# Kernel tuning notes

Hardware: AMD Instinct MI355X
Metric: run time of the kernel (lower is better)

Reference implementation:

```python
import jax, jax.numpy as jnp
import numpy as np


def _scan_dir(x, Wk, Wr, b):
    # x: (B,H,W,C) already flipped for the direction; Wk:(C,4U) Wr:(U,4U) b:(4U,)
    B, H, W, C = x.shape
    U = Wr.shape[0]
    Dmax = min(H, W)          # max anti-diagonal length
    D = H + W - 1             # number of anti-diagonals
    dt = x.dtype
    k = jnp.arange(Dmax)

    def step(carry, d):
        h1, c1, h2, c2 = carry            # diag d-1 and d-2 buffers, (B,Dmax,U)
        i0 = jnp.maximum(0, d - (W - 1))  # first row on diag d
        i1 = jnp.minimum(H - 1, d)        # last row on diag d
        rows = i0 + k
        cols = d - rows
        mask = rows <= i1                 # valid lanes on this diagonal
        rs = jnp.clip(rows, 0, H - 1)
        cs = jnp.clip(cols, 0, W - 1)
        x_diag = x[:, rs, cs, :]          # (B,Dmax,C)
        i0p = jnp.maximum(0, d - W)       # i0 of diag d-1
        i0pp = jnp.maximum(0, d - 1 - W)  # i0 of diag d-2

        def nb(buf, r_nb, lane0, extra):
            v = mask & extra
            lane = jnp.clip(r_nb - lane0, 0, Dmax - 1)
            g = jnp.take(buf, lane, axis=1)
            return jnp.where(v[None, :, None], g, jnp.zeros_like(g)), v

        up_ok = rows - 1 >= 0
        left_ok = cols - 1 >= 0
        h_up, v_up = nb(h1, rows - 1, i0p, up_ok)        # (i-1, j)   on diag d-1
        h_left, v_left = nb(h1, rows, i0p, left_ok)      # (i, j-1)   on diag d-1
        h_ul, v_ul = nb(h2, rows - 1, i0pp, up_ok & left_ok)  # (i-1,j-1) diag d-2
        c_up, _ = nb(c1, rows - 1, i0p, up_ok)
        c_left, _ = nb(c1, rows, i0p, left_ok)
        c_ul, _ = nb(c2, rows - 1, i0pp, up_ok & left_ok)

        cnt = (v_up.astype(dt) + v_left.astype(dt) + v_ul.astype(dt))[None, :, None]
        cnt = jnp.maximum(cnt, jnp.asarray(1.0, dt))
        h_prev = (h_up + h_left + h_ul) / cnt
        c_prev = (c_up + c_left + c_ul) / cnt

        # keras LSTMCell math, gate order i,f,g,o
        z = x_diag @ Wk + h_prev @ Wr + b
        zi, zf, zg, zo = jnp.split(z, 4, axis=-1)
        c_new = jax.nn.sigmoid(zf) * c_prev + jax.nn.sigmoid(zi) * jnp.tanh(zg)
        h_new = jax.nn.sigmoid(zo) * jnp.tanh(c_new)
        m = mask[None, :, None]
        h_new = jnp.where(m, h_new, jnp.zeros_like(h_new))
        c_new = jnp.where(m, c_new, jnp.zeros_like(c_new))
        return (h_new, c_new, h1, c1), h_new

    z0 = jnp.zeros((B, Dmax, U), dt)
    _, hs = jax.lax.scan(step, (z0, z0, z0, z0), jnp.arange(D))  # (D,B,Dmax,U)

    # scatter diagonal buffers back into the (B,H,W,U) grid (static indices)
    d_arr = np.arange(D)[:, None]
    kk = np.arange(Dmax)[None, :]
    rows_all = np.maximum(0, d_arr - (W - 1)) + kk
    cols_all = d_arr - rows_all
    valid = rows_all <= np.minimum(H - 1, d_arr)
    rws = np.where(valid, rows_all, H)   # invalid lanes -> padding row H
    cws = np.where(valid, cols_all, 0)
    out = jnp.zeros((B, H + 1, W, U), dt)
    out = out.at[:, rws, cws].set(jnp.transpose(hs, (1, 0, 2, 3)))
    return out[:, :H]


_FLIPS = [(False, False), (False, True), (True, False), (True, True)]  # SE,SW,NE,NW


def _forward(x, Wk, Wr, b):
    outs = []
    for i, (fh, fw) in enumerate(_FLIPS):
        xx = x
        if fh:
            xx = xx[:, ::-1]
        if fw:
            xx = xx[:, :, ::-1]
        o = _scan_dir(xx, Wk[i], Wr[i], b[i])
        if fw:
            o = o[:, :, ::-1]
        if fh:
            o = o[:, ::-1]
        outs.append(o)
    return jnp.concatenate(outs, axis=-1)


def setup_inputs() -> dict:
    key = jax.random.key(0)
    k0, k1, k2, k3 = jax.random.split(key, 4)
    B, H, W, C, U = 4, 128, 128, 64, 64
    x = jax.random.normal(k0, (B, H, W, C), jnp.float32)
    Wk = jax.random.normal(k1, (4, C, 4 * U), jnp.float32) * 0.08
    Wr = jax.random.normal(k2, (4, U, 4 * U), jnp.float32) * 0.08
    b = jax.random.normal(k3, (4, 4 * U), jnp.float32) * 0.02
    return {"x": x, "Wk": Wk, "Wr": Wr, "b": b}


def reference(x, Wk, Wr, b):
    return _forward(x, Wk, Wr, b)
```

## Files before the change

### kernel.cpp

```cpp
#include <hip/hip_runtime.h>

typedef __bf16 bf16x8 __attribute__((ext_vector_type(8)));
typedef __bf16 bf16x4 __attribute__((ext_vector_type(4)));
typedef float f32x4 __attribute__((ext_vector_type(4)));
typedef unsigned long long u64;

#define NCH 8
#define CELLS 16
#define NG 256
#define L2E 1.44269504089f
#define RDEPTH 16
#define NLINK (16 * 7)
#define RING_U64 (NLINK * RDEPTH * 64)
#define PROG_OFF (RING_U64 * 8)

__device__ __forceinline__ unsigned short f2bfbits(float f) {
  __bf16 b = (__bf16)f;
  return __builtin_bit_cast(unsigned short, b);
}
__device__ __forceinline__ float bfbits2f(unsigned short s) {
  return (float)__builtin_bit_cast(__bf16, s);
}
__device__ __forceinline__ void barrier_lds() {
  asm volatile("s_waitcnt lgkmcnt(0)" ::: "memory");
  __builtin_amdgcn_s_barrier();
}
__device__ __forceinline__ int hix(int row, int byteoff) {
  return row * 128 + (byteoff ^ ((row & 7) << 4));
}

__global__ __launch_bounds__(512, 1) void mdrnn_kernel(
    const float* __restrict__ x, const float* __restrict__ Wk,
    const float* __restrict__ Wr, const float* __restrict__ bias,
    float* __restrict__ out, char* __restrict__ ws) {
  __shared__ __align__(16) unsigned char xt[3][CELLS * 128];
  __shared__ __align__(16) unsigned char Pbuf[2][CELLS * 128];
  __shared__ __align__(16) unsigned char gbh[8 * 128];
  __shared__ __align__(16) float gbc[8 * 64];
  __shared__ __align__(16) float zbuf[2][4096];

  u64* __restrict__ ring = (u64*)ws;
  int* __restrict__ prog = (int*)(ws + PROG_OFF);

  const int tid = threadIdx.x;
  const bool isComp = (tid < 256);
  const int L = tid & 63;
  const int lo16 = L & 15;
  const int hi16 = L >> 4;
  const int wq = (tid >> 6) & 3;
  const int u = wq * 16 + lo16;
  const int hm0 = (tid >> 4) & 15;
  const int hq16 = tid & 15;

  const int ch = blockIdx.x >> 4;
  const int g = blockIdx.x & 15;
  const int f = g >> 2;
  const int bb = g & 3;
  const int fh = (f >> 1) & 1;
  const int fw = f & 1;
  const int R0 = ch * CELLS;
  const int D1 = R0 + 142;
  const int linkDn = g * 7 + ch - 1;
  const int linkUp = g * 7 + ch;

  for (int i = tid; i < 3 * CELLS * 32; i += 512) ((int*)xt)[i] = 0;
  for (int i = tid; i < 2 * CELLS * 32; i += 512) ((int*)Pbuf)[i] = 0;
  for (int i = tid; i < 8 * 32; i += 512) ((int*)gbh)[i] = 0;
  for (int i = tid; i < 8 * 64; i += 512) gbc[i] = 0.f;

  float bsc[4] = {0.f, 0.f, 0.f, 0.f};
  bf16x8 wkh[4][2], wrh[4][2], wrl[4][2];
  int oidx[4];
  int oStep = 0, cbase = 0;
  int o_ph0 = 0, o_ph1 = 0;
  int o_pw[4] = {0, 0, 0, 0};
  if (isComp) {
    const float* Wrf = Wr + f * (64 * NG);
#pragma unroll
    for (int t = 0; t < 4; ++t) {
      const float st = (t == 2) ? (2.f * L2E) : L2E;
#pragma unroll
      for (int kt = 0; kt < 2; ++kt)
#pragma unroll
        for (int jj = 0; jj < 8; ++jj) {
          int k = kt * 32 + hi16 * 8 + jj;
          float vr = Wrf[k * NG + t * 64 + u] * st;
          __bf16 vh = (__bf16)vr;
          wrh[t][kt][jj] = vh;
          wrl[t][kt][jj] = (__bf16)(vr - (float)vh);
        }
    }
    const int ccStep = fw ? -1 : 1;
#pragma unroll
    for (int j = 0; j < 4; ++j) {
      int ro = R0 + hi16 * 4 + j;
      int rr = fh ? 127 - ro : ro;
      int c0 = R0 - ro;
      oidx[j] = ((bb * 128 + rr) * 128 + (fw ? 127 - c0 : c0)) * NG + f * 64 + u;
      o_pw[j] = hix(hi16 * 4 + j, u * 2);
    }
    oStep = ccStep * NG;
    cbase = -hi16 * 4;
    o_ph0 = hix(lo16, hi16 * 16);
    o_ph1 = hix(lo16, 64 + hi16 * 16);
  } else {
    const float* Wkf = Wk + f * (64 * NG);
#pragma unroll
    for (int t = 0; t < 4; ++t) {
      const float st = (t == 2) ? (2.f * L2E) : L2E;
      bsc[t] = bias[f * NG + t * 64 + u] * st;
#pragma unroll
      for (int kt = 0; kt < 2; ++kt)
#pragma unroll
        for (int jj = 0; jj < 8; ++jj) {
          int k = kt * 32 + hi16 * 8 + jj;
          wkh[t][kt][jj] = (__bf16)(Wkf[k * NG + t * 64 + u] * st);
        }
    }
  }
  const int o_ax0 = hix(lo16, hi16 * 16);
  const int o_ax1 = hix(lo16, 64 + hi16 * 16);

  const int ccStepH = fw ? -1 : 1;
  const int rx = R0 + hm0;
  const int rrx = fh ? 127 - rx : rx;
  int cx = R0 - rx;
  int xidx = ((bb * 128 + rrx) * 128 + (fw ? 127 - cx : cx)) * 64 + hq16 * 4;
  const int xStep = ccStepH * 64;
  float4 px;
  bool pxv = false;
  auto ldg = [&]() {
    pxv = ((unsigned)cx <= 127u);
    px = make_float4(0.f, 0.f, 0.f, 0.f);
    if (pxv) px = *(const float4*)(x + xidx);
    xidx += xStep;
    ++cx;
  };
  auto stx = [&](unsigned char* buf) {
    if (pxv) {
      bf16x4 pk;
      pk[0] = (__bf16)px.x; pk[1] = (__bf16)px.y;
      pk[2] = (__bf16)px.z; pk[3] = (__bf16)px.w;
      *(bf16x4*)(buf + hix(hm0, hq16 * 8)) = pk;
    }
  };
  auto accx = [&](const unsigned char* xp, int bi) {
    bf16x8 a0 = *(const bf16x8*)(xp + o_ax0);
    bf16x8 a1 = *(const bf16x8*)(xp + o_ax1);
    float* zw = &zbuf[bi][0] + (wq * 64 + L) * 4;
#pragma unroll
    for (int t = 0; t < 4; ++t) {
      f32x4 az = (f32x4){bsc[t], bsc[t], bsc[t], bsc[t]};
      az = __builtin_amdgcn_mfma_f32_16x16x32_bf16(a0, wkh[t][0], az, 0, 0, 0);
      az = __builtin_amdgcn_mfma_f32_16x16x32_bf16(a1, wkh[t][1], az, 0, 0, 0);
      *(f32x4*)(zw + t * 1024) = az;
    }
  };

  __syncthreads();

  if (!isComp) {
    ldg();
    stx(&xt[R0 % 3][0]);
    ldg();
  }
  __syncthreads();

  if (!isComp) {
    stx(&xt[(R0 + 1) % 3][0]);
    ldg();
    accx(&xt[R0 % 3][0], R0 & 1);
    if (wq == 0 && ch > 0) {
#pragma unroll
      for (int k = 0; k < 2; ++k) {
        const int q = R0 - 1 + k;
        u64* src = ring + ((linkDn * RDEPTH + (q & (RDEPTH - 1))) << 6) + L;
        u64 v;
        int spin = 0;
        for (;;) {
          v = __hip_atomic_load(src, __ATOMIC_RELAXED, __HIP_MEMORY_SCOPE_AGENT);
          if ((unsigned short)(v >> 48) == (unsigned short)q ||
              spin >= (1 << 22))
            break;
          ++spin;
          __builtin_amdgcn_s_sleep(1);
        }
        *(unsigned short*)(gbh + (q & 7) * 128 + L * 2) =
            (unsigned short)(v >> 32);
        gbc[(q & 7) * 64 + L] = __uint_as_float((unsigned)v);
        if (k == 0)
          *(unsigned short*)(&Pbuf[(R0 + 1) & 1][0] + L * 2) =
              (unsigned short)(v >> 32);
      }
      if (L == 0)
        __hip_atomic_store(&prog[linkDn * 16], R0, __ATOMIC_RELAXED,
                           __HIP_MEMORY_SCOPE_AGENT);
    }
  }
  __syncthreads();

  f32x4 zacc[4];
  float hnprev[4];
  float csj[4];
  float puv[4];
  int gateSeen = 0;
  if (isComp) {
    const float* zb = &zbuf[R0 & 1][0] + (wq * 64 + L) * 4;
#pragma unroll
    for (int t = 0; t < 4; ++t) zacc[t] = *(const f32x4*)(zb + t * 1024);
    const float cu0 = gbc[((R0 - 1) & 7) * 64 + u];
#pragma unroll
    for (int j = 0; j < 4; ++j) {
      const float ci = (hi16 == 0 && j == 0) ? cu0 : 0.f;
      csj[j] = ci;
      puv[j] = ci;
      hnprev[j] = 0.f;
    }
    __builtin_amdgcn_s_setprio(1);
  } else {
    accx(&xt[(R0 + 1) % 3][0], (R0 + 1) & 1);
    stx(&xt[(R0 + 2) % 3][0]);
    ldg();
  }
  __syncthreads();

  unsigned char* Pc = &Pbuf[R0 & 1][0];
  unsigned char* Pp = &Pbuf[(R0 + 1) & 1][0];
  unsigned char* xA = &xt[(R0 + 2) % 3][0];
  unsigned char* xB = &xt[R0 % 3][0];
  unsigned char* xC = &xt[(R0 + 1) % 3][0];

  for (int d = R0; d <= D1; ++d) {
    if (isComp) {
      bf16x8 pa0 = *(const bf16x8*)(Pp + o_ph0);
      bf16x8 pa1 = *(const bf16x8*)(Pp + o_ph1);
      const float gh1 = bfbits2f(*(const unsigned short*)(gbh + (d & 7) * 128 + u * 2));
      const float gh2 = bfbits2f(*(const unsigned short*)(gbh + ((d - 1) & 7) * 128 + u * 2));
      const float gc1 = gbc[(d & 7) * 64 + u];
#pragma unroll
      for (int t = 0; t < 4; ++t)
        zacc[t] = __builtin_amdgcn_mfma_f32_16x16x32_bf16(pa0, wrh[t][0], zacc[t], 0, 0, 0);
#pragma unroll
      for (int t = 0; t < 4; ++t)
        zacc[t] = __builtin_amdgcn_mfma_f32_16x16x32_bf16(pa1, wrh[t][1], zacc[t], 0, 0, 0);
#pragma unroll
      for (int t = 0; t < 4; ++t)
        zacc[t] = __builtin_amdgcn_mfma_f32_16x16x32_bf16(pa0, wrl[t][0], zacc[t], 0, 0, 0);
#pragma unroll
      for (int t = 0; t < 4; ++t)
        zacc[t] = __builtin_amdgcn_mfma_f32_16x16x32_bf16(pa1, wrl[t][1], zacc[t], 0, 0, 0);

      const float* zbn = &zbuf[(d + 1) & 1][0] + (wq * 64 + L) * 4;
      const f32x4 znx0 = *(const f32x4*)(zbn);
      const f32x4 znx1 = *(const f32x4*)(zbn + 1024);
      const f32x4 znx2 = *(const f32x4*)(zbn + 2048);
      const f32x4 znx3 = *(const f32x4*)(zbn + 3072);

      const bool pubW = (ch < NCH - 1) && (d >= R0 + 15);

      float hcur[4], cnew[4];
      {
        const int cj = cbase - 3;
        const bool ok = ((unsigned)cj <= 127u);
        const float inv = (cj == 0) ? 1.f : (1.f / 3.f);
        const float cpj = csj[3] * inv;
        const float e1 = __builtin_amdgcn_exp2f(-zacc[1][3]);
        const float e2 = __builtin_amdgcn_exp2f(-zacc[0][3]);
        const float e3 = __builtin_amdgcn_exp2f(zacc[2][3]);
        const float A = 1.f + e1, Bv = 1.f + e2, Cv = 1.f + e3;
        const float BC = Bv * Cv;
        float cn = (cpj * BC + (e3 - 1.f) * A) *
                   __builtin_amdgcn_rcpf(A * BC);
        const float e4 = __builtin_amdgcn_exp2f(-zacc[3][3]);
        const float e5 = __builtin_amdgcn_exp2f(2.f * L2E * cn);
        float hn = (e5 - 1.f) * __builtin_amdgcn_rcpf((1.f + e4) * (1.f + e5));
        if (pubW && hi16 == 3) {
          u64 v = ((u64)(unsigned short)d << 48) | ((u64)f2bfbits(hn) << 32) |
                  (u64)__float_as_uint(cn);
          u64* dst = ring + ((linkUp * RDEPTH + (d & (RDEPTH - 1))) << 6) + u;
          __hip_atomic_store(dst, v, __ATOMIC_RELAXED,
                             __HIP_MEMORY_SCOPE_AGENT);
        }
        hcur[3] = ok ? hn : 0.f;
        cnew[3] = ok ? cn : 0.f;
      }
      const unsigned pk =
          ((unsigned)f2bfbits(hcur[3]) << 16) | f2bfbits(hnprev[3]);
      const unsigned pku = __shfl((int)pk, (L - 16) & 63);
      const float up_c = __shfl(cnew[3], (L - 16) & 63);
#pragma unroll
      for (int jj = 0; jj < 3; ++jj) {
        const int j = 2 - jj;
        const int cj = cbase - j;
        const bool ok = ((unsigned)cj <= 127u);
        const float inv =
            (cj == 0 || (j == 0 && R0 == 0 && hi16 == 0)) ? 1.f : (1.f / 3.f);
        const float cpj = csj[j] * inv;
        const float e1 = __builtin_amdgcn_exp2f(-zacc[1][j]);
        const float e2 = __builtin_amdgcn_exp2f(-zacc[0][j]);
        const float e3 = __builtin_amdgcn_exp2f(zacc[2][j]);
        const float A = 1.f + e1, Bv = 1.f + e2, Cv = 1.f + e3;
        const float BC = Bv * Cv;
        float cn = (cpj * BC + (e3 - 1.f) * A) *
                   __builtin_amdgcn_rcpf(A * BC);
        const float e4 = __builtin_amdgcn_exp2f(-zacc[3][j]);
        const float e5 = __builtin_amdgcn_exp2f(2.f * L2E * cn);
        float hn = (e5 - 1.f) * __builtin_amdgcn_rcpf((1.f + e4) * (1.f + e5));
        hcur[j] = ok ? hn : 0.f;
        cnew[j] = ok ? cn : 0.f;
      }
      const float up_h = bfbits2f((unsigned short)(pku >> 16));
      const float up_hp = bfbits2f((unsigned short)(pku & 0xffff));

#pragma unroll
      for (int j = 0; j < 4; ++j) {
        const float hup = j ? hcur[j - 1] : (hi16 ? up_h : gh1);
        const float hulp = j ? hnprev[j - 1] : (hi16 ? up_hp : gh2);
        const float sPj =
            ((cbase + 1 == j) || (R0 == 0 && hi16 == 0 && j == 0))
                ? 1.f : (1.f / 3.f);
        *(unsigned short*)(Pc + o_pw[j]) =
            f2bfbits(sPj * (hup + hcur[j] + hulp));
        const float cun = j ? cnew[j - 1] : (hi16 ? up_c : gc1);
        csj[j] = cun + cnew[j] + puv[j];
        puv[j] = cun;
      }
#pragma unroll
      for (int j = 0; j < 4; ++j) {
        if ((unsigned)(cbase - j) <= 127u) out[oidx[j]] = hcur[j];
        hnprev[j] = hcur[j];
        oidx[j] += oStep;
      }
      ++cbase;

      zacc[0] = znx0; zacc[1] = znx1; zacc[2] = znx2; zacc[3] = znx3;
    } else {
      const bool meAct = (ch > 0) && (wq == ((d - R0) & 1));
      const int q = d + 1;
      const bool qLive = meAct && (q >= R0 + 1) && (q <= R0 + 126);
      const u64* qs = ring + ((linkDn * RDEPTH + (q & (RDEPTH - 1))) << 6) + L;
      u64 qv = 0;
      if (qLive)
        qv = __hip_atomic_load(qs, __ATOMIC_RELAXED, __HIP_MEMORY_SCOPE_AGENT);
      const int nt = d + 1;
      const bool gatev = (wq == 2) && (ch < NCH - 1) && (nt <= D1) &&
                         (nt >= R0 + 15 + RDEPTH);
      int progNow = gateSeen;
      if (gatev && gateSeen < nt - RDEPTH)
        progNow = __hip_atomic_load(&prog[linkUp * 16], __ATOMIC_RELAXED,
                                    __HIP_MEMORY_SCOPE_AGENT);

      accx(xA, (d + 2) & 1);
      stx(xB);
      ldg();

      if (qLive) {
        int spin = 0;
        while ((unsigned short)(qv >> 48) != (unsigned short)q &&
               spin < (1 << 22)) {
          ++spin;
          __builtin_amdgcn_s_sleep(1);
          qv = __hip_atomic_load(qs, __ATOMIC_RELAXED,
                                 __HIP_MEMORY_SCOPE_AGENT);
        }
        *(unsigned short*)(gbh + (q & 7) * 128 + L * 2) =
            (unsigned short)(qv >> 32);
        gbc[(q & 7) * 64 + L] = __uint_as_float((unsigned)qv);
      }
      if (meAct && L == 0)
        __hip_atomic_store(&prog[linkDn * 16], min(d + 1, R0 + 126),
                           __ATOMIC_RELAXED, __HIP_MEMORY_SCOPE_AGENT);
      if (gatev) {
        if (progNow > gateSeen) gateSeen = progNow;
        int spin = 0;
        while (gateSeen < nt - RDEPTH && spin < (1 << 22)) {
          ++spin;
          __builtin_amdgcn_s_sleep(1);
          gateSeen = __hip_atomic_load(&prog[linkUp * 16], __ATOMIC_RELAXED,
                                       __HIP_MEMORY_SCOPE_AGENT);
        }
      }
    }

    {
      unsigned char* t0 = xA; xA = xB; xB = xC; xC = t0;
      unsigned char* t1 = Pc; Pc = Pp; Pp = t1;
    }
    barrier_lds();
  }
}

extern "C" void kernel_launch(void* const* d_in, const int* in_sizes, int n_in,
                              void* d_out, int out_size, void* d_ws, size_t ws_size,
                              hipStream_t stream) {
  const float* x = (const float*)d_in[0];
  const float* Wk = (const float*)d_in[1];
  const float* Wr = (const float*)d_in[2];
  const float* b = (const float*)d_in[3];
  float* out = (float*)d_out;
  hipMemsetAsync(d_ws, 0, PROG_OFF + NLINK * 16 * sizeof(int), stream);
  hipLaunchKernelGGL(mdrnn_kernel, dim3(128), dim3(512), 0, stream, x, Wk, Wr,
                     b, out, (char*)d_ws);
}
```

Before: 225.8 us.

## Move input-projection MFMAs into compute warps and drop LDS z buffer

The x@Wk input projection was computed by the helper (loader) warps and handed to the compute warps through a double-buffered 32KB LDS z buffer. Now the compute warps hold the Wk weights and bias themselves and issue the projection MFMAs for the next diagonal at the end of each step, reading x tiles directly from LDS. This removes the z-buffer LDS writes and reads and frees shared memory. In exchange it adds 8 MFMAs and more register pressure to the latency-critical recurrent path.

```diff
diff --git a/kernel.cpp b/kernel.cpp
--- a/kernel.cpp
+++ b/kernel.cpp
@@ -37,7 +37,6 @@
   __shared__ __align__(16) unsigned char Pbuf[2][CELLS * 128];
   __shared__ __align__(16) unsigned char gbh[8 * 128];
   __shared__ __align__(16) float gbc[8 * 64];
-  __shared__ __align__(16) float zbuf[2][4096];
 
   u64* __restrict__ ring = (u64*)ws;
   int* __restrict__ prog = (int*)(ws + PROG_OFF);
@@ -76,9 +75,11 @@
   int o_pw[4] = {0, 0, 0, 0};
   if (isComp) {
     const float* Wrf = Wr + f * (64 * NG);
+    const float* Wkf = Wk + f * (64 * NG);
 #pragma unroll
     for (int t = 0; t < 4; ++t) {
       const float st = (t == 2) ? (2.f * L2E) : L2E;
+      bsc[t] = bias[f * NG + t * 64 + u] * st;
 #pragma unroll
       for (int kt = 0; kt < 2; ++kt)
 #pragma unroll
@@ -88,6 +89,7 @@
           __bf16 vh = (__bf16)vr;
           wrh[t][kt][jj] = vh;
           wrl[t][kt][jj] = (__bf16)(vr - (float)vh);
+          wkh[t][kt][jj] = (__bf16)(Wkf[k * NG + t * 64 + u] * st);
         }
     }
     const int ccStep = fw ? -1 : 1;
@@ -103,20 +105,6 @@
     cbase = -hi16 * 4;
     o_ph0 = hix(lo16, hi16 * 16);
     o_ph1 = hix(lo16, 64 + hi16 * 16);
-  } else {
-    const float* Wkf = Wk + f * (64 * NG);
-#pragma unroll
-    for (int t = 0; t < 4; ++t) {
-      const float st = (t == 2) ? (2.f * L2E) : L2E;
-      bsc[t] = bias[f * NG + t * 64 + u] * st;
-#pragma unroll
-      for (int kt = 0; kt < 2; ++kt)
-#pragma unroll
-        for (int jj = 0; jj < 8; ++jj) {
-          int k = kt * 32 + hi16 * 8 + jj;
-          wkh[t][kt][jj] = (__bf16)(Wkf[k * NG + t * 64 + u] * st);
-        }
-    }
   }
   const int o_ax0 = hix(lo16, hi16 * 16);
   const int o_ax1 = hix(lo16, 64 + hi16 * 16);
@@ -144,18 +132,6 @@
       *(bf16x4*)(buf + hix(hm0, hq16 * 8)) = pk;
     }
   };
-  auto accx = [&](const unsigned char* xp, int bi) {
-    bf16x8 a0 = *(const bf16x8*)(xp + o_ax0);
-    bf16x8 a1 = *(const bf16x8*)(xp + o_ax1);
-    float* zw = &zbuf[bi][0] + (wq * 64 + L) * 4;
-#pragma unroll
-    for (int t = 0; t < 4; ++t) {
-      f32x4 az = (f32x4){bsc[t], bsc[t], bsc[t], bsc[t]};
-      az = __builtin_amdgcn_mfma_f32_16x16x32_bf16(a0, wkh[t][0], az, 0, 0, 0);
-      az = __builtin_amdgcn_mfma_f32_16x16x32_bf16(a1, wkh[t][1], az, 0, 0, 0);
-      *(f32x4*)(zw + t * 1024) = az;
-    }
-  };
 
   __syncthreads();
 
@@ -169,7 +145,6 @@
   if (!isComp) {
     stx(&xt[(R0 + 1) % 3][0]);
     ldg();
-    accx(&xt[R0 % 3][0], R0 & 1);
     if (wq == 0 && ch > 0) {
 #pragma unroll
       for (int k = 0; k < 2; ++k) {
@@ -205,9 +180,15 @@
   float puv[4];
   int gateSeen = 0;
   if (isComp) {
-    const float* zb = &zbuf[R0 & 1][0] + (wq * 64 + L) * 4;
-#pragma unroll
-    for (int t = 0; t < 4; ++t) zacc[t] = *(const f32x4*)(zb + t * 1024);
+    const unsigned char* xp = &xt[R0 % 3][0];
+    bf16x8 a0 = *(const bf16x8*)(xp + o_ax0);
+    bf16x8 a1 = *(const bf16x8*)(xp + o_ax1);
+#pragma unroll
+    for (int t = 0; t < 4; ++t) {
+      zacc[t] = (f32x4){bsc[t], bsc[t], bsc[t], bsc[t]};
+      zacc[t] = __builtin_amdgcn_mfma_f32_16x16x32_bf16(a0, wkh[t][0], zacc[t], 0, 0, 0);
+      zacc[t] = __builtin_amdgcn_mfma_f32_16x16x32_bf16(a1, wkh[t][1], zacc[t], 0, 0, 0);
+    }
     const float cu0 = gbc[((R0 - 1) & 7) * 64 + u];
 #pragma unroll
     for (int j = 0; j < 4; ++j) {
@@ -218,7 +199,6 @@
     }
     __builtin_amdgcn_s_setprio(1);
   } else {
-    accx(&xt[(R0 + 1) % 3][0], (R0 + 1) & 1);
     stx(&xt[(R0 + 2) % 3][0]);
     ldg();
   }
@@ -234,6 +214,8 @@
     if (isComp) {
       bf16x8 pa0 = *(const bf16x8*)(Pp + o_ph0);
       bf16x8 pa1 = *(const bf16x8*)(Pp + o_ph1);
+      bf16x8 a0 = *(const bf16x8*)(xC + o_ax0);
+      bf16x8 a1 = *(const bf16x8*)(xC + o_ax1);
       const float gh1 = bfbits2f(*(const unsigned short*)(gbh + (d & 7) * 128 + u * 2));
       const float gh2 = bfbits2f(*(const unsigned short*)(gbh + ((d - 1) & 7) * 128 + u * 2));
       const float gc1 = gbc[(d & 7) * 64 + u];
@@ -249,12 +231,6 @@
 #pragma unroll
       for (int t = 0; t < 4; ++t)
         zacc[t] = __builtin_amdgcn_mfma_f32_16x16x32_bf16(pa1, wrl[t][1], zacc[t], 0, 0, 0);
-
-      const float* zbn = &zbuf[(d + 1) & 1][0] + (wq * 64 + L) * 4;
-      const f32x4 znx0 = *(const f32x4*)(zbn);
-      const f32x4 znx1 = *(const f32x4*)(zbn + 1024);
-      const f32x4 znx2 = *(const f32x4*)(zbn + 2048);
-      const f32x4 znx3 = *(const f32x4*)(zbn + 3072);
 
       const bool pubW = (ch < NCH - 1) && (d >= R0 + 15);
 
@@ -333,7 +309,12 @@
       }
       ++cbase;
 
-      zacc[0] = znx0; zacc[1] = znx1; zacc[2] = znx2; zacc[3] = znx3;
+#pragma unroll
+      for (int t = 0; t < 4; ++t) {
+        zacc[t] = (f32x4){bsc[t], bsc[t], bsc[t], bsc[t]};
+        zacc[t] = __builtin_amdgcn_mfma_f32_16x16x32_bf16(a0, wkh[t][0], zacc[t], 0, 0, 0);
+        zacc[t] = __builtin_amdgcn_mfma_f32_16x16x32_bf16(a1, wkh[t][1], zacc[t], 0, 0, 0);
+      }
     } else {
       const bool meAct = (ch > 0) && (wq == ((d - R0) & 1));
       const int q = d + 1;
@@ -350,7 +331,6 @@
         progNow = __hip_atomic_load(&prog[linkUp * 16], __ATOMIC_RELAXED,
                                     __HIP_MEMORY_SCOPE_AGENT);
 
-      accx(xA, (d + 2) & 1);
       stx(xB);
       ldg();
 
```

Measured after the change: 222.9 us, median of 2. No clear change (-1.3%).
